# Kernel tuning notes

Hardware: AMD Instinct MI355X
Metric: run time of the kernel (lower is better)

Reference implementation:

```python
import jax, jax.numpy as jnp
import numpy as np

# fHOG orientation lookup (cos/sin of k*20 degrees), exactly the hardcoded
# constants used in Felzenszwalb's features.cc / mmcv extract_hog kernel.
UU = jnp.array([1.0000, 0.9397, 0.7660, 0.5000, 0.1736,
                -0.1736, -0.5000, -0.7660, -0.9397], dtype=jnp.float32)
VV = jnp.array([0.0000, 0.3420, 0.6428, 0.8660, 0.9848,
                0.9848, 0.8660, 0.6428, 0.3420], dtype=jnp.float32)
EPS = 1e-4


def _hog(img, sbin):
    B, C, H, W = img.shape
    bh = int(round(H / sbin)); bw = int(round(W / sbin))
    vh, vw = bh * sbin, bw * sbin
    # central differences at pixels (1..visible-2), source index clamped to dim-2
    ys = jnp.clip(jnp.arange(1, vh - 1), 0, H - 2)
    xs = jnp.clip(jnp.arange(1, vw - 1), 0, W - 2)
    dy = img[:, :, ys + 1][:, :, :, xs] - img[:, :, ys - 1][:, :, :, xs]
    dx = img[:, :, ys][:, :, :, xs + 1] - img[:, :, ys][:, :, :, xs - 1]
    v = dx * dx + dy * dy                      # [B,3,hg,wg]
    ch = jnp.argmax(v, axis=1, keepdims=True)  # channel with max gradient energy
    dxs = jnp.take_along_axis(dx, ch, axis=1)[:, 0]
    dys = jnp.take_along_axis(dy, ch, axis=1)[:, 0]
    mag = jnp.sqrt(dxs * dxs + dys * dys)      # [B,hg,wg]
    # snap to one of 18 signed orientations
    dot = UU[None, :, None, None] * dxs[:, None] + VV[None, :, None, None] * dys[:, None]
    best_o = jnp.argmax(jnp.concatenate([dot, -dot], axis=1), axis=1)  # [B,hg,wg]
    # bilinear spatial soft-binning into sbin x sbin cells
    yp = (jnp.arange(1, vh - 1, dtype=img.dtype) + 0.5) / sbin - 0.5
    xp = (jnp.arange(1, vw - 1, dtype=img.dtype) + 0.5) / sbin - 0.5
    iyp = jnp.floor(yp).astype(jnp.int32); ixp = jnp.floor(xp).astype(jnp.int32)
    vy0 = yp - iyp; vx0 = xp - ixp; vy1 = 1.0 - vy0; vx1 = 1.0 - vx0
    hg, wg = vh - 2, vw - 2
    bidx = jnp.arange(B)[:, None, None]
    IY = jnp.broadcast_to(iyp[None, :, None], (B, hg, wg))
    IX = jnp.broadcast_to(ixp[None, None, :], (B, hg, wg))
    WY0 = vy0[None, :, None]; WY1 = vy1[None, :, None]
    WX0 = vx0[None, None, :]; WX1 = vx1[None, None, :]
    hist = jnp.zeros((B, 18, bh, bw), dtype=img.dtype)

    def scat(h, iy, ix, w):
        valid = (iy >= 0) & (iy < bh) & (ix >= 0) & (ix < bw)
        iyc = jnp.clip(iy, 0, bh - 1); ixc = jnp.clip(ix, 0, bw - 1)
        return h.at[bidx, best_o, iyc, ixc].add(jnp.where(valid, w * mag, 0.0))

    hist = scat(hist, IY, IX, WY1 * WX1)
    hist = scat(hist, IY, IX + 1, WY1 * WX0)
    hist = scat(hist, IY + 1, IX, WY0 * WX1)
    hist = scat(hist, IY + 1, IX + 1, WY0 * WX0)
    # cell energy from contrast-insensitive sums
    s = hist[:, :9] + hist[:, 9:]
    norm = jnp.sum(s * s, axis=1)              # [B,bh,bw]
    # 2x2 block sums of norm
    T = norm[:, :-1, :-1] + norm[:, 1:, :-1] + norm[:, :-1, 1:] + norm[:, 1:, 1:]
    n1 = jax.lax.rsqrt(T[:, 1:, 1:] + EPS)[:, None]
    n2 = jax.lax.rsqrt(T[:, :-1, 1:] + EPS)[:, None]
    n3 = jax.lax.rsqrt(T[:, 1:, :-1] + EPS)[:, None]
    n4 = jax.lax.rsqrt(T[:, :-1, :-1] + EPS)[:, None]
    src = hist[:, :, 1:-1, 1:-1]               # [B,18,oh,ow]
    h1 = jnp.minimum(src * n1, 0.2); h2 = jnp.minimum(src * n2, 0.2)
    h3 = jnp.minimum(src * n3, 0.2); h4 = jnp.minimum(src * n4, 0.2)
    f_cs = 0.5 * (h1 + h2 + h3 + h4)           # 18 contrast-sensitive feats
    ss = src[:, :9] + src[:, 9:]
    f_ci = 0.5 * (jnp.minimum(ss * n1, 0.2) + jnp.minimum(ss * n2, 0.2)
                  + jnp.minimum(ss * n3, 0.2) + jnp.minimum(ss * n4, 0.2))
    tex = 0.2357 * jnp.stack([h1.sum(1), h2.sum(1), h3.sum(1), h4.sum(1)], axis=1)
    feat = jnp.concatenate([f_cs, f_ci, tex], axis=1)  # [B,31,oh,ow]
    return jnp.pad(feat, ((0, 0), (0, 0), (1, 1), (1, 1)))


def setup_inputs() -> dict:
    key = jax.random.key(0)
    img = jax.random.uniform(key, (16, 3, 512, 512), dtype=jnp.float32)
    return {"input": img, "sbin": 4}


def reference(input, sbin):
    return _hog(input, sbin)
```

## Files before the change

### kernel.cpp

```cpp
#include <hip/hip_runtime.h>

#define BATCH 16
#define CHN 3
#define H 512
#define W 512
#define BH 128
#define BW 128
#define HG 510
#define WG 510

__global__ __launch_bounds__(256) void hog_grad(const float* __restrict__ img,
                                                float* __restrict__ mag,
                                                unsigned char* __restrict__ obuf)
{
    int x = blockIdx.x * 64 + threadIdx.x;
    int y = blockIdx.y * 4 + threadIdx.y;
    int b = blockIdx.z;
    if (x >= WG || y >= HG) return;
    int py = y + 1, px = x + 1;

    const float* im = img + (size_t)b * CHN * H * W;
    float bestv = -1.0f, bdx = 0.0f, bdy = 0.0f;
#pragma unroll
    for (int c = 0; c < CHN; c++) {
        const float* p = im + (size_t)c * H * W;
        float dyv = __fsub_rn(p[(size_t)(py + 1) * W + px], p[(size_t)(py - 1) * W + px]);
        float dxv = __fsub_rn(p[(size_t)py * W + px + 1], p[(size_t)py * W + px - 1]);
        float v = __fadd_rn(__fmul_rn(dxv, dxv), __fmul_rn(dyv, dyv));
        if (v > bestv) { bestv = v; bdx = dxv; bdy = dyv; }
    }
    float mg = __fsqrt_rn(bestv);

    const float uu[9] = {1.0f, 0.9397f, 0.766f, 0.5f, 0.1736f, -0.1736f, -0.5f, -0.766f, -0.9397f};
    const float vvt[9] = {0.0f, 0.342f, 0.6428f, 0.866f, 0.9848f, 0.9848f, 0.866f, 0.6428f, 0.342f};
    float d[9];
#pragma unroll
    for (int o = 0; o < 9; o++)
        d[o] = __fadd_rn(__fmul_rn(uu[o], bdx), __fmul_rn(vvt[o], bdy));
    float best = -1e30f; int bo = 0;
#pragma unroll
    for (int o = 0; o < 9; o++) { if (d[o] > best) { best = d[o]; bo = o; } }
#pragma unroll
    for (int o = 0; o < 9; o++) { float nd = -d[o]; if (nd > best) { best = nd; bo = o + 9; } }

    size_t idx = ((size_t)b * HG + y) * WG + x;
    mag[idx] = mg;
    obuf[idx] = (unsigned char)bo;
}

__global__ __launch_bounds__(256) void hog_hist(const float* __restrict__ mag,
                                                const unsigned char* __restrict__ obuf,
                                                float* __restrict__ hist,
                                                float* __restrict__ nrm)
{
    __shared__ float hl[18 * 256];
    int cx = threadIdx.x;
    int cy = blockIdx.y * 2 + threadIdx.y;
    int b = blockIdx.z;
    int t = threadIdx.y * 128 + cx;

#pragma unroll
    for (int o = 0; o < 18; o++) hl[o * 256 + t] = 0.0f;

    const float wt[8] = {0.125f, 0.375f, 0.625f, 0.875f, 0.875f, 0.625f, 0.375f, 0.125f};
    const float* mb = mag + (size_t)b * HG * WG;
    const unsigned char* ob = obuf + (size_t)b * HG * WG;
    int ry0 = 4 * cy - 3;
    int rx0 = 4 * cx - 3;

#pragma unroll
    for (int ky = 0; ky < 8; ky++) {
        int ry = ry0 + ky;
        if ((unsigned)ry >= (unsigned)HG) continue;
        float wy = wt[ky];
        const float* mr = mb + (size_t)ry * WG;
        const unsigned char* orr = ob + (size_t)ry * WG;
#pragma unroll
        for (int kx = 0; kx < 8; kx++) {
            int rx = rx0 + kx;
            if ((unsigned)rx >= (unsigned)WG) continue;
            float m = mr[rx];
            int o = orr[rx];
            hl[o * 256 + t] += (wy * wt[kx]) * m;
        }
    }

    float h[18];
#pragma unroll
    for (int o = 0; o < 18; o++) {
        h[o] = hl[o * 256 + t];
        hist[(((size_t)b * 18 + o) * BH + cy) * BW + cx] = h[o];
    }
    float s = 0.0f;
#pragma unroll
    for (int o = 0; o < 9; o++) { float ss = h[o] + h[o + 9]; s += ss * ss; }
    nrm[((size_t)b * BH + cy) * BW + cx] = s;
}

__global__ __launch_bounds__(256) void hog_feat(const float* __restrict__ hist,
                                                const float* __restrict__ nrm,
                                                float* __restrict__ out)
{
    int ox = threadIdx.x;
    int oy = blockIdx.y * 2 + threadIdx.y;
    int b = blockIdx.z;

    if (ox == 0 || ox == BW - 1 || oy == 0 || oy == BH - 1) {
#pragma unroll
        for (int c = 0; c < 31; c++)
            out[(((size_t)b * 31 + c) * BH + oy) * BW + ox] = 0.0f;
        return;
    }

    const float* nb = nrm + (size_t)b * BH * BW;
    float n00 = nb[(size_t)(oy - 1) * BW + ox - 1], n01 = nb[(size_t)(oy - 1) * BW + ox], n02 = nb[(size_t)(oy - 1) * BW + ox + 1];
    float n10 = nb[(size_t)oy * BW + ox - 1],       n11 = nb[(size_t)oy * BW + ox],       n12 = nb[(size_t)oy * BW + ox + 1];
    float n20 = nb[(size_t)(oy + 1) * BW + ox - 1], n21 = nb[(size_t)(oy + 1) * BW + ox], n22 = nb[(size_t)(oy + 1) * BW + ox + 1];

    float T11 = n11 + n21 + n12 + n22;
    float T01 = n01 + n11 + n02 + n12;
    float T10 = n10 + n20 + n11 + n21;
    float T00 = n00 + n10 + n01 + n11;
    float v1 = 1.0f / __fsqrt_rn(T11 + 1e-4f);
    float v2 = 1.0f / __fsqrt_rn(T01 + 1e-4f);
    float v3 = 1.0f / __fsqrt_rn(T10 + 1e-4f);
    float v4 = 1.0f / __fsqrt_rn(T00 + 1e-4f);

    float h[18];
#pragma unroll
    for (int o = 0; o < 18; o++)
        h[o] = hist[(((size_t)b * 18 + o) * BH + oy) * BW + ox];

    float t1 = 0.f, t2 = 0.f, t3 = 0.f, t4 = 0.f;
#pragma unroll
    for (int o = 0; o < 18; o++) {
        float s = h[o];
        float a1 = fminf(s * v1, 0.2f);
        float a2 = fminf(s * v2, 0.2f);
        float a3 = fminf(s * v3, 0.2f);
        float a4 = fminf(s * v4, 0.2f);
        out[(((size_t)b * 31 + o) * BH + oy) * BW + ox] = 0.5f * (a1 + a2 + a3 + a4);
        t1 += a1; t2 += a2; t3 += a3; t4 += a4;
    }
#pragma unroll
    for (int o = 0; o < 9; o++) {
        float ss = h[o] + h[o + 9];
        float a1 = fminf(ss * v1, 0.2f);
        float a2 = fminf(ss * v2, 0.2f);
        float a3 = fminf(ss * v3, 0.2f);
        float a4 = fminf(ss * v4, 0.2f);
        out[(((size_t)b * 31 + 18 + o) * BH + oy) * BW + ox] = 0.5f * (a1 + a2 + a3 + a4);
    }
    out[(((size_t)b * 31 + 27) * BH + oy) * BW + ox] = 0.2357f * t1;
    out[(((size_t)b * 31 + 28) * BH + oy) * BW + ox] = 0.2357f * t2;
    out[(((size_t)b * 31 + 29) * BH + oy) * BW + ox] = 0.2357f * t3;
    out[(((size_t)b * 31 + 30) * BH + oy) * BW + ox] = 0.2357f * t4;
}

extern "C" void kernel_launch(void* const* d_in, const int* in_sizes, int n_in,
                              void* d_out, int out_size, void* d_ws, size_t ws_size,
                              hipStream_t stream)
{
    const float* img = (const float*)d_in[0];
    float* out = (float*)d_out;
    char* ws = (char*)d_ws;

    float* mag          = (float*)ws;
    unsigned char* obuf = (unsigned char*)(ws + 16646400);
    float* hist         = (float*)(ws + 20808000);
    float* nrm          = (float*)(ws + 39682368);

    dim3 b1(64, 4, 1), g1((WG + 63) / 64, (HG + 3) / 4, BATCH);
    hog_grad<<<g1, b1, 0, stream>>>(img, mag, obuf);

    dim3 b2(128, 2, 1), g2(1, BH / 2, BATCH);
    hog_hist<<<g2, b2, 0, stream>>>(mag, obuf, hist, nrm);
    hog_feat<<<g2, b2, 0, stream>>>(hist, nrm, out);
}
```

Baseline: 134.7 us.

## Pack magnitude and orientation into one word and vectorize gradient and histogram loads

The gradient kernel now handles four pixels per thread using float4 row loads. It packs the magnitude, with its low 5 mantissa bits cleared, together with the 5-bit orientation index into a single uint per pixel, stored in a row-padded (512-wide) buffer. The histogram kernel reads this packed buffer with aligned uint4 loads and unrolls its 8-tap window explicitly, instead of gathering separate float and byte arrays. The aim is to cut intermediate memory traffic and the number of load instructions. The cost is a small precision loss in magnitude from mantissa truncation, plus some tail-handling complexity.

```diff
diff --git a/kernel.cpp b/kernel.cpp
--- a/kernel.cpp
+++ b/kernel.cpp
@@ -1,55 +1,98 @@
 #include <hip/hip_runtime.h>
 
 #define BATCH 16
-#define CHN 3
 #define H 512
 #define W 512
 #define BH 128
 #define BW 128
 #define HG 510
 #define WG 510
+#define PKW 512
+
 
 __global__ __launch_bounds__(256) void hog_grad(const float* __restrict__ img,
-                                                float* __restrict__ mag,
-                                                unsigned char* __restrict__ obuf)
-{
-    int x = blockIdx.x * 64 + threadIdx.x;
-    int y = blockIdx.y * 4 + threadIdx.y;
-    int b = blockIdx.z;
-    if (x >= WG || y >= HG) return;
-    int py = y + 1, px = x + 1;
-
-    const float* im = img + (size_t)b * CHN * H * W;
-    float bestv = -1.0f, bdx = 0.0f, bdy = 0.0f;
-#pragma unroll
-    for (int c = 0; c < CHN; c++) {
-        const float* p = im + (size_t)c * H * W;
-        float dyv = __fsub_rn(p[(size_t)(py + 1) * W + px], p[(size_t)(py - 1) * W + px]);
-        float dxv = __fsub_rn(p[(size_t)py * W + px + 1], p[(size_t)py * W + px - 1]);
-        float v = __fadd_rn(__fmul_rn(dxv, dxv), __fmul_rn(dyv, dyv));
-        if (v > bestv) { bestv = v; bdx = dxv; bdy = dyv; }
-    }
-    float mg = __fsqrt_rn(bestv);
+                                                unsigned int* __restrict__ pk)
+{
+    int tx = threadIdx.x;
+    int gx = blockIdx.x * 64 + tx;
+    int y  = blockIdx.y * 4 + threadIdx.y;
+    int b  = blockIdx.z;
+    if (y >= HG) return;
+    int x0 = gx * 4;
+    bool tail = (x0 == 508);
+    int w0 = tail ? 504 : x0;
+    int py = y + 1;
+
+    const float* im = img + (size_t)b * 3 * H * W;
+
+    float bv0 = -1.f, bv1 = -1.f, bv2 = -1.f, bv3 = -1.f;
+    float bx0 = 0, bx1 = 0, bx2 = 0, bx3 = 0;
+    float by0 = 0, by1 = 0, by2 = 0, by3 = 0;
+
+#pragma unroll
+    for (int c = 0; c < 3; c++) {
+        const float* base = im + (size_t)c * H * W;
+        const float* rm = base + (size_t)(py - 1) * W + w0;
+        const float* rc = base + (size_t)py * W + w0;
+        const float* rp = base + (size_t)(py + 1) * W + w0;
+        float4 ma = *(const float4*)rm, mb = *(const float4*)(rm + 4);
+        float4 ca = *(const float4*)rc, cb = *(const float4*)(rc + 4);
+        float4 pa = *(const float4*)rp, pb = *(const float4*)(rp + 4);
+        float M1 = tail ? mb.y : ma.y, M2 = tail ? mb.z : ma.z;
+        float M3 = tail ? mb.w : ma.w, M4 = tail ? mb.w : mb.x;
+        float P1 = tail ? pb.y : pa.y, P2 = tail ? pb.z : pa.z;
+        float P3 = tail ? pb.w : pa.w, P4 = tail ? pb.w : pb.x;
+        float C0 = tail ? cb.x : ca.x, C1 = tail ? cb.y : ca.y;
+        float C2 = tail ? cb.z : ca.z, C3 = tail ? cb.w : ca.w;
+        float C4 = tail ? cb.w : cb.x, C5 = tail ? cb.w : cb.y;
+
+        float dx0 = __fsub_rn(C2, C0), dx1 = __fsub_rn(C3, C1);
+        float dx2 = __fsub_rn(C4, C2), dx3 = __fsub_rn(C5, C3);
+        float dy0 = __fsub_rn(P1, M1), dy1 = __fsub_rn(P2, M2);
+        float dy2 = __fsub_rn(P3, M3), dy3 = __fsub_rn(P4, M4);
+
+        float v0 = __fadd_rn(__fmul_rn(dx0, dx0), __fmul_rn(dy0, dy0));
+        float v1 = __fadd_rn(__fmul_rn(dx1, dx1), __fmul_rn(dy1, dy1));
+        float v2 = __fadd_rn(__fmul_rn(dx2, dx2), __fmul_rn(dy2, dy2));
+        float v3 = __fadd_rn(__fmul_rn(dx3, dx3), __fmul_rn(dy3, dy3));
+        if (v0 > bv0) { bv0 = v0; bx0 = dx0; by0 = dy0; }
+        if (v1 > bv1) { bv1 = v1; bx1 = dx1; by1 = dy1; }
+        if (v2 > bv2) { bv2 = v2; bx2 = dx2; by2 = dy2; }
+        if (v3 > bv3) { bv3 = v3; bx3 = dx3; by3 = dy3; }
+    }
 
     const float uu[9] = {1.0f, 0.9397f, 0.766f, 0.5f, 0.1736f, -0.1736f, -0.5f, -0.766f, -0.9397f};
-    const float vvt[9] = {0.0f, 0.342f, 0.6428f, 0.866f, 0.9848f, 0.9848f, 0.866f, 0.6428f, 0.342f};
-    float d[9];
-#pragma unroll
-    for (int o = 0; o < 9; o++)
-        d[o] = __fadd_rn(__fmul_rn(uu[o], bdx), __fmul_rn(vvt[o], bdy));
-    float best = -1e30f; int bo = 0;
-#pragma unroll
-    for (int o = 0; o < 9; o++) { if (d[o] > best) { best = d[o]; bo = o; } }
-#pragma unroll
-    for (int o = 0; o < 9; o++) { float nd = -d[o]; if (nd > best) { best = nd; bo = o + 9; } }
-
-    size_t idx = ((size_t)b * HG + y) * WG + x;
-    mag[idx] = mg;
-    obuf[idx] = (unsigned char)bo;
-}
-
-__global__ __launch_bounds__(256) void hog_hist(const float* __restrict__ mag,
-                                                const unsigned char* __restrict__ obuf,
+    const float vv[9] = {0.0f, 0.342f, 0.6428f, 0.866f, 0.9848f, 0.9848f, 0.866f, 0.6428f, 0.342f};
+
+    unsigned int pkv[4];
+    float bvv[4] = {bv0, bv1, bv2, bv3};
+    float bxx[4] = {bx0, bx1, bx2, bx3};
+    float byy[4] = {by0, by1, by2, by3};
+#pragma unroll
+    for (int i = 0; i < 4; i++) {
+        float mg = __fsqrt_rn(bvv[i]);
+        float best = -1e30f; int bo = 0;
+#pragma unroll
+        for (int o = 0; o < 9; o++) {
+            float d = __fadd_rn(__fmul_rn(uu[o], bxx[i]), __fmul_rn(vv[o], byy[i]));
+            if (d > best) { best = d; bo = o; }
+            float nd = -d;
+            (void)nd;
+        }
+#pragma unroll
+        for (int o = 0; o < 9; o++) {
+            float d = __fadd_rn(__fmul_rn(uu[o], bxx[i]), __fmul_rn(vv[o], byy[i]));
+            float nd = -d;
+            if (nd > best) { best = nd; bo = o + 9; }
+        }
+        unsigned int v = (__float_as_uint(mg) & 0xFFFFFFE0u) | (unsigned int)bo;
+        pkv[i] = (x0 + i < WG) ? v : 0u;
+    }
+    uint4 o4 = make_uint4(pkv[0], pkv[1], pkv[2], pkv[3]);
+    *(uint4*)(pk + ((size_t)b * HG + y) * PKW + x0) = o4;
+}
+
+__global__ __launch_bounds__(256) void hog_hist(const unsigned int* __restrict__ pk,
                                                 float* __restrict__ hist,
                                                 float* __restrict__ nrm)
 {
@@ -63,25 +106,33 @@
     for (int o = 0; o < 18; o++) hl[o * 256 + t] = 0.0f;
 
     const float wt[8] = {0.125f, 0.375f, 0.625f, 0.875f, 0.875f, 0.625f, 0.375f, 0.125f};
-    const float* mb = mag + (size_t)b * HG * WG;
-    const unsigned char* ob = obuf + (size_t)b * HG * WG;
+    const float wl[4] = {0.0f, 0.125f, 0.375f, 0.625f};
+    const float wm[4] = {0.875f, 0.875f, 0.625f, 0.375f};
+
+    const unsigned int* pb = pk + (size_t)b * HG * PKW;
     int ry0 = 4 * cy - 3;
-    int rx0 = 4 * cx - 3;
+    int xb = 4 * cx;
 
 #pragma unroll
     for (int ky = 0; ky < 8; ky++) {
         int ry = ry0 + ky;
         if ((unsigned)ry >= (unsigned)HG) continue;
         float wy = wt[ky];
-        const float* mr = mb + (size_t)ry * WG;
-        const unsigned char* orr = ob + (size_t)ry * WG;
-#pragma unroll
-        for (int kx = 0; kx < 8; kx++) {
-            int rx = rx0 + kx;
-            if ((unsigned)rx >= (unsigned)WG) continue;
-            float m = mr[rx];
-            int o = orr[rx];
-            hl[o * 256 + t] += (wy * wt[kx]) * m;
+        const unsigned int* row = pb + (size_t)ry * PKW;
+        if (cx > 0) {
+            uint4 L = *(const uint4*)(row + xb - 4);
+            { unsigned p = L.y; hl[(p & 31u) * 256 + t] += (wy * wl[1]) * __uint_as_float(p & 0xFFFFFFE0u); }
+            { unsigned p = L.z; hl[(p & 31u) * 256 + t] += (wy * wl[2]) * __uint_as_float(p & 0xFFFFFFE0u); }
+            { unsigned p = L.w; hl[(p & 31u) * 256 + t] += (wy * wl[3]) * __uint_as_float(p & 0xFFFFFFE0u); }
+        }
+        uint4 M = *(const uint4*)(row + xb);
+        { unsigned p = M.x; hl[(p & 31u) * 256 + t] += (wy * wm[0]) * __uint_as_float(p & 0xFFFFFFE0u); }
+        { unsigned p = M.y; hl[(p & 31u) * 256 + t] += (wy * wm[1]) * __uint_as_float(p & 0xFFFFFFE0u); }
+        if (cx < 127) {
+            { unsigned p = M.z; hl[(p & 31u) * 256 + t] += (wy * wm[2]) * __uint_as_float(p & 0xFFFFFFE0u); }
+            { unsigned p = M.w; hl[(p & 31u) * 256 + t] += (wy * wm[3]) * __uint_as_float(p & 0xFFFFFFE0u); }
+            unsigned p = row[xb + 4];
+            hl[(p & 31u) * 256 + t] += (wy * 0.125f) * __uint_as_float(p & 0xFFFFFFE0u);
         }
     }
 
@@ -165,15 +216,14 @@
     float* out = (float*)d_out;
     char* ws = (char*)d_ws;
 
-    float* mag          = (float*)ws;
-    unsigned char* obuf = (unsigned char*)(ws + 16646400);
-    float* hist         = (float*)(ws + 20808000);
-    float* nrm          = (float*)(ws + 39682368);
-
-    dim3 b1(64, 4, 1), g1((WG + 63) / 64, (HG + 3) / 4, BATCH);
-    hog_grad<<<g1, b1, 0, stream>>>(img, mag, obuf);
+    unsigned int* pk = (unsigned int*)ws;
+    float* hist      = (float*)(ws + 16715776);
+    float* nrm       = (float*)(ws + 35590144);
+
+    dim3 b1(64, 4, 1), g1(2, 128, BATCH);
+    hog_grad<<<g1, b1, 0, stream>>>(img, pk);
 
     dim3 b2(128, 2, 1), g2(1, BH / 2, BATCH);
-    hog_hist<<<g2, b2, 0, stream>>>(mag, obuf, hist, nrm);
+    hog_hist<<<g2, b2, 0, stream>>>(pk, hist, nrm);
     hog_feat<<<g2, b2, 0, stream>>>(hist, nrm, out);
 }
```

Result: faster. 120.5 us (-10.6%).
